# Optimization experiments

Measured on AMD Instinct MI355X. Metric: run time of the kernel, lower is better.

The kernel has to match this reference:

```python
import jax, jax.numpy as jnp
import numpy as np
import math

RANK = 396

def setup_inputs() -> dict:
    key = jax.random.key(0)
    ks = jax.random.split(key, 8)
    batch, L, wemb, temb, tags, rank = 16, 128, 400, 20, 25, RANK
    std = 0.1545
    return {
        "word_emb": jax.random.normal(ks[0], (batch, L, wemb), dtype=jnp.float32),
        "tag_emd": jax.random.normal(ks[1], (tags, temb), dtype=jnp.float32),
        "W1": jax.random.normal(ks[2], (wemb, rank), dtype=jnp.float32) * std,
        "W2": jax.random.normal(ks[3], (wemb, rank), dtype=jnp.float32) * std,
        "W3": jax.random.normal(ks[4], (wemb, rank), dtype=jnp.float32) * std,
        "T1": jax.random.normal(ks[5], (temb, rank), dtype=jnp.float32) * std,
        "T2": jax.random.normal(ks[6], (temb, rank), dtype=jnp.float32) * std,
        "T3": jax.random.normal(ks[7], (temb, rank), dtype=jnp.float32) * std,
    }

def reference(word_emb, tag_emd, W1, W2, W3, T1, T2, T3):
    # word_emb: [n, L, wemb]; output: [n, L-2, tags, tags, tags]
    g1 = word_emb[:, :-2] @ W1   # [n, m, k]
    g2 = word_emb[:, 1:-1] @ W2
    g3 = word_emb[:, 2:] @ W3
    g4 = tag_emd @ T1            # [a, k]
    g5 = tag_emd @ T2
    g6 = tag_emd @ T3
    temp01 = g1 * g2 * g3                               # [n, m, k]
    temp02 = jnp.einsum('ak,bk,ck->abck', g4, g5, g6)   # [a, b, c, k]
    score = jnp.einsum('nmk,abck->nmabc', temp01, temp02)
    score = score / jnp.asarray(math.sqrt(RANK), score.dtype)
    return score
```

## Files before the change

kernel.cpp:

```cpp
#include <hip/hip_runtime.h>
#include <hip/hip_bf16.h>
#include <stdint.h>

#define KP    416
#define RANKD 396
#define WEMB  400
#define TEMB  20
#define TAGS  25
#define BATCH 16
#define LSEQ  128
#define MROWS 126
#define NM    2016
#define NMP   2048
#define ABC   15625
#define ABCP  15744
#define SCALE 0.050251890762960605f

typedef __attribute__((ext_vector_type(8))) short short8;
typedef __attribute__((ext_vector_type(4))) float f32x4;

#define OFF_T01  0
#define OFF_T02  1703936
#define OFF_WORD 14802944
#define OFF_WT   16506880
#define OFF_G    17545216

#define GLOAD_LDS16(gp, lp) \
  __builtin_amdgcn_global_load_lds((const __attribute__((address_space(1))) uint32_t*)(gp), \
                                   (__attribute__((address_space(3))) uint32_t*)(lp), 16, 0, 0)

__device__ __forceinline__ uint16_t f2bf(float f) {
    union { float f; uint32_t u; } v; v.f = f;
    uint32_t u = v.u;
    return (uint16_t)((u + 0x7FFFu + ((u >> 16) & 1u)) >> 16);
}

#define J1_BLK 3328
#define J2_BLK 2028
#define J3_BLK 122
__global__ void k_prep(const float* __restrict__ word,
                       const float* __restrict__ W1, const float* __restrict__ W2,
                       const float* __restrict__ W3, const float* __restrict__ tag,
                       const float* __restrict__ T1, const float* __restrict__ T2,
                       const float* __restrict__ T3,
                       uint16_t* __restrict__ wordb, uint16_t* __restrict__ wt,
                       float* __restrict__ g) {
    int bx = blockIdx.x;
    if (bx < J1_BLK) {
        int idx = bx * 256 + threadIdx.x;
        int e = idx % KP, row = idx / KP;
        wordb[idx] = f2bf((e < WEMB) ? word[row * WEMB + e] : 0.f);
    } else if (bx < J1_BLK + J2_BLK) {
        int idx = (bx - J1_BLK) * 256 + threadIdx.x;
        int j = idx / (KP * KP);
        int rem = idx % (KP * KP);
        int k = rem / KP, e = rem % KP;
        const float* W = (j == 0) ? W1 : (j == 1) ? W2 : W3;
        wt[idx] = f2bf((k < RANKD && e < WEMB) ? W[e * RANKD + k] : 0.f);
    } else {
        int idx = (bx - J1_BLK - J2_BLK) * 256 + threadIdx.x;
        if (idx >= 3 * TAGS * KP) return;
        int j = idx / (TAGS * KP);
        int rem = idx % (TAGS * KP);
        int a = rem / KP, k = rem % KP;
        const float* T = (j == 0) ? T1 : (j == 1) ? T2 : T3;
        float s = 0.f;
        if (k < RANKD) {
            for (int e = 0; e < TEMB; ++e) s += tag[a * TEMB + e] * T[e * RANKD + k];
        }
        g[idx] = s;
    }
}

#define T01_BLK 896
#define T02_BLK 3198
__global__ __launch_bounds__(256) void k_mid(const uint16_t* __restrict__ word,
                                             const uint16_t* __restrict__ wt,
                                             const float* __restrict__ g,
                                             uint16_t* __restrict__ t01,
                                             uint16_t* __restrict__ t02) {
    int bx = blockIdx.x;
    if (bx < T01_BLK) {
        int wid = threadIdx.x >> 6, lane = threadIdx.x & 63;
        int nmtile = bx & 127;
        int ktile = (bx >> 7) * 4 + wid;
        if (ktile >= KP / 16) return;
        int col_l = lane & 15, kblk = lane >> 4;
        int colk = ktile * 16 + col_l;
        f32x4 acc1 = {0.f, 0.f, 0.f, 0.f}, acc2 = acc1, acc3 = acc1;
        if (nmtile < NM / 16) {
            int nm_a = nmtile * 16 + col_l;
            int n = nm_a / MROWS, m = nm_a % MROWS;
            const uint16_t* arow = word + (size_t)(n * LSEQ + m) * KP;
            const uint16_t* b1 = wt + (size_t)colk * KP;
            const uint16_t* b2 = wt + (size_t)KP * KP + (size_t)colk * KP;
            const uint16_t* b3 = wt + (size_t)2 * KP * KP + (size_t)colk * KP;
            for (int e0 = 0; e0 < KP; e0 += 32) {
                int eo = e0 + kblk * 8;
                short8 a0 = *(const short8*)(arow + eo);
                short8 a1 = *(const short8*)(arow + KP + eo);
                short8 a2 = *(const short8*)(arow + 2 * KP + eo);
                short8 v1 = *(const short8*)(b1 + eo);
                short8 v2 = *(const short8*)(b2 + eo);
                short8 v3 = *(const short8*)(b3 + eo);
                acc1 = __builtin_amdgcn_mfma_f32_16x16x32_bf16(a0, v1, acc1, 0, 0, 0);
                acc2 = __builtin_amdgcn_mfma_f32_16x16x32_bf16(a1, v2, acc2, 0, 0, 0);
                acc3 = __builtin_amdgcn_mfma_f32_16x16x32_bf16(a2, v3, acc3, 0, 0, 0);
            }
        }
        for (int r = 0; r < 4; ++r) {
            int row = nmtile * 16 + kblk * 4 + r;
            float v = acc1[r] * acc2[r] * acc3[r] * SCALE;
            t01[(size_t)row * KP + colk] = f2bf(v);
        }
    } else {
        int idx = (bx - T01_BLK) * 256 + threadIdx.x;
        int abc = idx / (KP / 8), kc = idx % (KP / 8);
        int k0 = kc * 8;
        short8 o;
        if (abc < ABC) {
            int a = abc / 625, rem = abc % 625, b = rem / 25, c = rem % 25;
            const float4* ga = (const float4*)(g + (size_t)a * KP + k0);
            const float4* gb = (const float4*)(g + (size_t)TAGS * KP + (size_t)b * KP + k0);
            const float4* gc = (const float4*)(g + (size_t)2 * TAGS * KP + (size_t)c * KP + k0);
            float4 a0 = ga[0], a1 = ga[1];
            float4 b0 = gb[0], b1 = gb[1];
            float4 c0 = gc[0], c1 = gc[1];
            o[0] = (short)f2bf(a0.x * b0.x * c0.x);
            o[1] = (short)f2bf(a0.y * b0.y * c0.y);
            o[2] = (short)f2bf(a0.z * b0.z * c0.z);
            o[3] = (short)f2bf(a0.w * b0.w * c0.w);
            o[4] = (short)f2bf(a1.x * b1.x * c1.x);
            o[5] = (short)f2bf(a1.y * b1.y * c1.y);
            o[6] = (short)f2bf(a1.z * b1.z * c1.z);
            o[7] = (short)f2bf(a1.w * b1.w * c1.w);
        } else {
            for (int t = 0; t < 8; ++t) o[t] = 0;
        }
        *(short8*)(t02 + (size_t)abc * KP + k0) = o;
    }
}

__global__ __launch_bounds__(256) void k_final(const uint16_t* __restrict__ t01,
                                               const uint16_t* __restrict__ t02,
                                               float* __restrict__ out) {
    __shared__ uint16_t lds[2][2][128 * 32];
    int tid = threadIdx.x;
    int wid = tid >> 6, lane = tid & 63;
    int col_l = lane & 15, kblk = lane >> 4;
    int brow = blockIdx.x * 128, bcol = blockIdx.y * 128;
    int wrow = (wid >> 1) * 64, wcol = (wid & 1) * 64;

    int off0 = wid * 1024;
    int off1 = (wid + 4) * 1024;
    int by0 = off0 + lane * 16, by1 = off1 + lane * 16;
    int r0 = by0 >> 6, ks0 = (by0 >> 4) & 3;
    int r1 = by1 >> 6, ks1 = (by1 >> 4) & 3;

    const uint16_t* ga0 = t01 + (size_t)(brow + r0) * KP + ks0 * 8;
    const uint16_t* ga1 = t01 + (size_t)(brow + r1) * KP + ks1 * 8;
    const uint16_t* gb0 = t02 + (size_t)(bcol + r0) * KP + ks0 * 8;
    const uint16_t* gb1 = t02 + (size_t)(bcol + r1) * KP + ks1 * 8;

    f32x4 acc[4][4];
#pragma unroll
    for (int i = 0; i < 4; ++i)
#pragma unroll
        for (int j = 0; j < 4; ++j)
            acc[i][j] = (f32x4){0.f, 0.f, 0.f, 0.f};

    auto stage = [&](int buf, int kk) {
        GLOAD_LDS16(ga0 + kk, &lds[buf][0][off0 >> 1]);
        GLOAD_LDS16(ga1 + kk, &lds[buf][0][off1 >> 1]);
        GLOAD_LDS16(gb0 + kk, &lds[buf][1][off0 >> 1]);
        GLOAD_LDS16(gb1 + kk, &lds[buf][1][off1 >> 1]);
    };

    const int NT = KP / 32;
    stage(0, 0);
    for (int kt = 0; kt < NT; ++kt) {
        int cur = kt & 1;
        if (kt + 1 < NT) stage(cur ^ 1, (kt + 1) * 32);
        __syncthreads();
        const uint16_t* la = &lds[cur][0][0];
        const uint16_t* lb = &lds[cur][1][0];
        short8 a[4], b[4];
#pragma unroll
        for (int i = 0; i < 4; ++i)
            a[i] = *(const short8*)(la + (wrow + i * 16 + col_l) * 32 + kblk * 8);
#pragma unroll
        for (int j = 0; j < 4; ++j)
            b[j] = *(const short8*)(lb + (wcol + j * 16 + col_l) * 32 + kblk * 8);
#pragma unroll
        for (int i = 0; i < 4; ++i)
#pragma unroll
            for (int j = 0; j < 4; ++j)
                acc[i][j] = __builtin_amdgcn_mfma_f32_16x16x32_bf16(a[i], b[j], acc[i][j], 0, 0, 0);
        __syncthreads();
    }

#pragma unroll
    for (int i = 0; i < 4; ++i) {
        int row_b = brow + wrow + i * 16 + kblk * 4;
#pragma unroll
        for (int j = 0; j < 4; ++j) {
            int col = bcol + wcol + j * 16 + col_l;
            if (col >= ABC) continue;
#pragma unroll
            for (int r = 0; r < 4; ++r) {
                int row = row_b + r;
                if (row < NM) out[(size_t)row * ABC + col] = acc[i][j][r];
            }
        }
    }
}

extern "C" void kernel_launch(void* const* d_in, const int* in_sizes, int n_in,
                              void* d_out, int out_size, void* d_ws, size_t ws_size,
                              hipStream_t stream) {
    const float* word = (const float*)d_in[0];
    const float* tag  = (const float*)d_in[1];
    const float* W1   = (const float*)d_in[2];
    const float* W2   = (const float*)d_in[3];
    const float* W3   = (const float*)d_in[4];
    const float* T1   = (const float*)d_in[5];
    const float* T2   = (const float*)d_in[6];
    const float* T3   = (const float*)d_in[7];
    float* out = (float*)d_out;
    char* ws = (char*)d_ws;

    uint16_t* t01   = (uint16_t*)(ws + OFF_T01);
    uint16_t* t02   = (uint16_t*)(ws + OFF_T02);
    uint16_t* wordb = (uint16_t*)(ws + OFF_WORD);
    uint16_t* wt    = (uint16_t*)(ws + OFF_WT);
    float*    g     = (float*)(ws + OFF_G);

    k_prep<<<J1_BLK + J2_BLK + J3_BLK, 256, 0, stream>>>(word, W1, W2, W3, tag,
                                                         T1, T2, T3, wordb, wt, g);
    k_mid<<<T01_BLK + T02_BLK, 256, 0, stream>>>(wordb, wt, g, t01, t02);
    k_final<<<dim3(NMP / 128, ABCP / 128), 256, 0, stream>>>(t01, t02, out);
}
```

Before: 87.90 us.

## Rewrite final GEMM with 256x256 tiles, 4-stage LDS pipeline and block swizzle

Replaces the 128x128 double-buffered final GEMM with a 512-thread, 256x256-tile kernel. It uses a 4-deep LDS ring buffer prefetching three k-steps ahead, splits each k-step into two MFMA halves with barriers and s_setprio, and swizzles block IDs for L2 locality. ABC padding grows to a multiple of 256, with workspace offsets and the k_mid block count adjusted to match. This aims to raise MFMA utilization and hide global latency, at the cost of more wasted padded columns and higher register and LDS pressure.

After: 102.7 us. 16.8% more time.

```diff
diff --git a/kernel.cpp b/kernel.cpp
--- a/kernel.cpp
+++ b/kernel.cpp
@@ -13,7 +13,7 @@
 #define NM    2016
 #define NMP   2048
 #define ABC   15625
-#define ABCP  15744
+#define ABCP  15872
 #define SCALE 0.050251890762960605f
 
 typedef __attribute__((ext_vector_type(8))) short short8;
@@ -21,9 +21,9 @@
 
 #define OFF_T01  0
 #define OFF_T02  1703936
-#define OFF_WORD 14802944
-#define OFF_WT   16506880
-#define OFF_G    17545216
+#define OFF_WORD 14909440
+#define OFF_WT   16613376
+#define OFF_G    17651712
 
 #define GLOAD_LDS16(gp, lp) \
   __builtin_amdgcn_global_load_lds((const __attribute__((address_space(1))) uint32_t*)(gp), \
@@ -73,7 +73,7 @@
 }
 
 #define T01_BLK 896
-#define T02_BLK 3198
+#define T02_BLK 3224
 __global__ __launch_bounds__(256) void k_mid(const uint16_t* __restrict__ word,
                                              const uint16_t* __restrict__ wt,
                                              const float* __restrict__ g,
@@ -141,75 +141,114 @@
     }
 }
 
-__global__ __launch_bounds__(256) void k_final(const uint16_t* __restrict__ t01,
-                                               const uint16_t* __restrict__ t02,
-                                               float* __restrict__ out) {
-    __shared__ uint16_t lds[2][2][128 * 32];
-    int tid = threadIdx.x;
-    int wid = tid >> 6, lane = tid & 63;
-    int col_l = lane & 15, kblk = lane >> 4;
-    int brow = blockIdx.x * 128, bcol = blockIdx.y * 128;
-    int wrow = (wid >> 1) * 64, wcol = (wid & 1) * 64;
-
-    int off0 = wid * 1024;
-    int off1 = (wid + 4) * 1024;
-    int by0 = off0 + lane * 16, by1 = off1 + lane * 16;
-    int r0 = by0 >> 6, ks0 = (by0 >> 4) & 3;
-    int r1 = by1 >> 6, ks1 = (by1 >> 4) & 3;
-
-    const uint16_t* ga0 = t01 + (size_t)(brow + r0) * KP + ks0 * 8;
-    const uint16_t* ga1 = t01 + (size_t)(brow + r1) * KP + ks1 * 8;
-    const uint16_t* gb0 = t02 + (size_t)(bcol + r0) * KP + ks0 * 8;
-    const uint16_t* gb1 = t02 + (size_t)(bcol + r1) * KP + ks1 * 8;
-
-    f32x4 acc[4][4];
-#pragma unroll
-    for (int i = 0; i < 4; ++i)
-#pragma unroll
-        for (int j = 0; j < 4; ++j)
-            acc[i][j] = (f32x4){0.f, 0.f, 0.f, 0.f};
-
-    auto stage = [&](int buf, int kk) {
-        GLOAD_LDS16(ga0 + kk, &lds[buf][0][off0 >> 1]);
-        GLOAD_LDS16(ga1 + kk, &lds[buf][0][off1 >> 1]);
-        GLOAD_LDS16(gb0 + kk, &lds[buf][1][off0 >> 1]);
-        GLOAD_LDS16(gb1 + kk, &lds[buf][1][off1 >> 1]);
-    };
+__global__ __launch_bounds__(512, 2) void k_final(const uint16_t* __restrict__ t01,
+                                                  const uint16_t* __restrict__ t02,
+                                                  float* __restrict__ out) {
+    __shared__ __align__(16) uint16_t ldsA[4][8192];
+    __shared__ __align__(16) uint16_t ldsB[4][8192];
+    const int tid = threadIdx.x;
+    const int wid = tid >> 6, lane = tid & 63;
+    const int col_l = lane & 15, kblk = lane >> 4;
+
+    const int bid = blockIdx.x;
+    const int swz = (bid & 7) * 62 + (bid >> 3);
+    const int mb = swz & 7, nb = swz >> 3;
+    const int brow = mb * 256, bcol = nb * 256;
+
+    const int wrow = (wid >> 2) * 128, wcol = (wid & 3) * 64;
+
+    const int rowS = tid & 255, ksS = tid >> 8;
+    const uint16_t* gA0 = t01 + (size_t)(brow + rowS) * KP + ksS * 8;
+    const uint16_t* gA1 = gA0 + 16;
+    const uint16_t* gB0 = t02 + (size_t)(bcol + rowS) * KP + ksS * 8;
+    const uint16_t* gB1 = gB0 + 16;
+    const int c0 = wid * 512;
+    const int c1 = 4096 + wid * 512;
+
+    f32x4 acc[8][4];
+#pragma unroll
+    for (int m = 0; m < 8; ++m)
+#pragma unroll
+        for (int n = 0; n < 4; ++n)
+            acc[m][n] = (f32x4){0.f, 0.f, 0.f, 0.f};
+
+#pragma unroll
+    for (int t = 0; t < 3; ++t) {
+        GLOAD_LDS16(gA0 + t * 32, &ldsA[t][c0]);
+        GLOAD_LDS16(gA1 + t * 32, &ldsA[t][c1]);
+        GLOAD_LDS16(gB0 + t * 32, &ldsB[t][c0]);
+        GLOAD_LDS16(gB1 + t * 32, &ldsB[t][c1]);
+    }
+    asm volatile("s_waitcnt vmcnt(8)" ::: "memory");
+    __builtin_amdgcn_s_barrier();
 
     const int NT = KP / 32;
-    stage(0, 0);
+#pragma unroll
     for (int kt = 0; kt < NT; ++kt) {
-        int cur = kt & 1;
-        if (kt + 1 < NT) stage(cur ^ 1, (kt + 1) * 32);
-        __syncthreads();
-        const uint16_t* la = &lds[cur][0][0];
-        const uint16_t* lb = &lds[cur][1][0];
-        short8 a[4], b[4];
-#pragma unroll
-        for (int i = 0; i < 4; ++i)
-            a[i] = *(const short8*)(la + (wrow + i * 16 + col_l) * 32 + kblk * 8);
-#pragma unroll
-        for (int j = 0; j < 4; ++j)
-            b[j] = *(const short8*)(lb + (wcol + j * 16 + col_l) * 32 + kblk * 8);
-#pragma unroll
-        for (int i = 0; i < 4; ++i)
-#pragma unroll
-            for (int j = 0; j < 4; ++j)
-                acc[i][j] = __builtin_amdgcn_mfma_f32_16x16x32_bf16(a[i], b[j], acc[i][j], 0, 0, 0);
-        __syncthreads();
-    }
-
-#pragma unroll
-    for (int i = 0; i < 4; ++i) {
-        int row_b = brow + wrow + i * 16 + kblk * 4;
-#pragma unroll
-        for (int j = 0; j < 4; ++j) {
-            int col = bcol + wcol + j * 16 + col_l;
-            if (col >= ABC) continue;
-#pragma unroll
-            for (int r = 0; r < 4; ++r) {
-                int row = row_b + r;
-                if (row < NM) out[(size_t)row * ABC + col] = acc[i][j][r];
+        const int buf = kt & 3, nbuf = (kt + 3) & 3;
+        const uint16_t* bA = ldsA[buf];
+        const uint16_t* bB = ldsB[buf];
+        const bool st = (kt + 3) < NT;
+
+        short8 bF[4], aF[4];
+#pragma unroll
+        for (int n = 0; n < 4; ++n)
+            bF[n] = *(const short8*)(bB + kblk * 2048 + (wcol + n * 16 + col_l) * 8);
+#pragma unroll
+        for (int m = 0; m < 4; ++m)
+            aF[m] = *(const short8*)(bA + kblk * 2048 + (wrow + m * 16 + col_l) * 8);
+        if (st) {
+            GLOAD_LDS16(gA0 + (kt + 3) * 32, &ldsA[nbuf][c0]);
+            GLOAD_LDS16(gA1 + (kt + 3) * 32, &ldsA[nbuf][c1]);
+        }
+        __builtin_amdgcn_s_barrier();
+        asm volatile("s_waitcnt lgkmcnt(0)" ::: "memory");
+        __builtin_amdgcn_sched_barrier(0);
+        __builtin_amdgcn_s_setprio(1);
+#pragma unroll
+        for (int m = 0; m < 4; ++m)
+#pragma unroll
+            for (int n = 0; n < 4; ++n)
+                acc[m][n] = __builtin_amdgcn_mfma_f32_16x16x32_bf16(aF[m], bF[n], acc[m][n], 0, 0, 0);
+        __builtin_amdgcn_s_setprio(0);
+        __builtin_amdgcn_s_barrier();
+
+        short8 aG[4];
+#pragma unroll
+        for (int m = 0; m < 4; ++m)
+            aG[m] = *(const short8*)(bA + kblk * 2048 + (wrow + (m + 4) * 16 + col_l) * 8);
+        if (st) {
+            GLOAD_LDS16(gB0 + (kt + 3) * 32, &ldsB[nbuf][c0]);
+            GLOAD_LDS16(gB1 + (kt + 3) * 32, &ldsB[nbuf][c1]);
+        }
+        __builtin_amdgcn_s_barrier();
+        asm volatile("s_waitcnt lgkmcnt(0)" ::: "memory");
+        __builtin_amdgcn_sched_barrier(0);
+        __builtin_amdgcn_s_setprio(1);
+#pragma unroll
+        for (int m = 0; m < 4; ++m)
+#pragma unroll
+            for (int n = 0; n < 4; ++n)
+                acc[m + 4][n] = __builtin_amdgcn_mfma_f32_16x16x32_bf16(aG[m], bF[n], acc[m + 4][n], 0, 0, 0);
+        __builtin_amdgcn_s_setprio(0);
+        if (kt <= NT - 4)      { asm volatile("s_waitcnt vmcnt(8)" ::: "memory"); }
+        else if (kt == NT - 3) { asm volatile("s_waitcnt vmcnt(4)" ::: "memory"); }
+        else if (kt == NT - 2) { asm volatile("s_waitcnt vmcnt(0)" ::: "memory"); }
+        if (kt < NT - 1) __builtin_amdgcn_s_barrier();
+    }
+
+#pragma unroll
+    for (int m = 0; m < 8; ++m) {
+        int row_b = brow + wrow + m * 16 + kblk * 4;
+#pragma unroll
+        for (int n = 0; n < 4; ++n) {
+            int col = bcol + wcol + n * 16 + col_l;
+            if (col < ABC) {
+#pragma unroll
+                for (int r = 0; r < 4; ++r) {
+                    int row = row_b + r;
+                    if (row < NM) out[(size_t)row * ABC + col] = acc[m][n][r];
+                }
             }
         }
     }
@@ -238,5 +277,5 @@
     k_prep<<<J1_BLK + J2_BLK + J3_BLK, 256, 0, stream>>>(word, W1, W2, W3, tag,
                                                          T1, T2, T3, wordb, wt, g);
     k_mid<<<T01_BLK + T02_BLK, 256, 0, stream>>>(wordb, wt, g, t01, t02);
-    k_final<<<dim3(NMP / 128, ABCP / 128), 256, 0, stream>>>(t01, t02, out);
-}
+    k_final<<<NMP / 256 * (ABCP / 256), 512, 0, stream>>>(t01, t02, out);
+}
```
